# Performance work log

Measured on AMD Instinct MI355X. Metric: run time of the kernel, lower is better.

## Reference

```python
import jax, jax.numpy as jnp
import numpy as np

B, T, H, V = 32, 256, 1024, 256


def setup_inputs() -> dict:
    key = jax.random.key(0)
    ks = jax.random.split(key, 12)
    xavier = float(np.sqrt(6.0 / (H + V)))
    inp = {
        "x": jax.random.randint(ks[0], (B, T), 0, V, dtype=jnp.int64),
        "targets": jax.random.randint(ks[1], (B, T), 0, V, dtype=jnp.int64),
        "h0": jnp.zeros((B, H), jnp.float32),
        "c0": jnp.zeros((B, H), jnp.float32),
        "h1": jnp.zeros((B, H), jnp.float32),
        "c1": jnp.zeros((B, H), jnp.float32),
        # learned params
        "emb": jax.random.normal(ks[2], (V, H), jnp.float32) * 0.05,
        "W_ih0": jax.random.normal(ks[3], (H, 4 * H), jnp.float32) / np.sqrt(H),
        "W_hh0": jax.random.normal(ks[4], (H, 4 * H), jnp.float32) / np.sqrt(H),
        "b0": jnp.zeros((4 * H,), jnp.float32),
        "W_ih1": jax.random.normal(ks[5], (H, 4 * H), jnp.float32) / np.sqrt(H),
        "W_hh1": jax.random.normal(ks[6], (H, 4 * H), jnp.float32) / np.sqrt(H),
        "b1": jnp.zeros((4 * H,), jnp.float32),
        "W_out": jax.random.uniform(ks[7], (H, V), jnp.float32, -xavier, xavier),
        "b_out": jnp.zeros((V,), jnp.float32),
    }
    return inp


def _lstm_cell(h, c, inp, W_ih, W_hh, b):
    # gates: [B, 4H] -> i, f, g, o
    z = inp @ W_ih + h @ W_hh + b
    i, f, g, o = jnp.split(z, 4, axis=-1)
    c_new = jax.nn.sigmoid(f) * c + jax.nn.sigmoid(i) * jnp.tanh(g)
    h_new = jax.nn.sigmoid(o) * jnp.tanh(c_new)
    return h_new, c_new


def reference(x, targets, h0, c0, h1, c1, emb, W_ih0, W_hh0, b0,
              W_ih1, W_hh1, b1, W_out, b_out):
    # Teacher-forcing branch: embed targets, feed embedding at every step.
    embeddings = emb[targets]            # [B, T, H]
    e_seq = jnp.swapaxes(embeddings, 0, 1)  # [T, B, H] for scan over time

    def step(carry, e_t):
        (h0, c0), (h1, c1) = carry
        h0, c0 = _lstm_cell(h0, c0, e_t, W_ih0, W_hh0, b0)
        h1, c1 = _lstm_cell(h1, c1, h0, W_ih1, W_hh1, b1)
        logit = h1 @ W_out + b_out       # [B, V]
        return ((h0, c0), (h1, c1)), logit

    carry0 = ((h0, c0), (h1, c1))
    carry_f, logits_tbv = jax.lax.scan(step, carry0, e_seq)
    logits = jnp.swapaxes(logits_tbv, 0, 1)  # [B, T, V]
    (h0f, c0f), (h1f, c1f) = carry_f
    return logits, h0f, c0f, h1f, c1f
```

## Files before the change

### kernel.cpp

```cpp
#include <hip/hip_runtime.h>
#include <cstdint>


typedef float  f32x4 __attribute__((ext_vector_type(4)));
typedef short  s16x8 __attribute__((ext_vector_type(8)));

#define DEV __device__ __forceinline__

DEV unsigned short f2bf(float x){
  unsigned u = __builtin_bit_cast(unsigned, x);
  unsigned r = (u + 0x7fffu + ((u >> 16) & 1u)) >> 16;
  return (unsigned short)r;
}
DEV float bf2f(unsigned short b){ return __builtin_bit_cast(float, ((unsigned)b) << 16); }

DEV s16x8 ld16(const void* p){ return *(const s16x8*)p; }

DEV f32x4 MF(s16x8 a, s16x8 b, f32x4 c){
  return __builtin_amdgcn_mfma_f32_16x16x32_bf16(a, b, c, 0, 0, 0);
}

#define LDC(dst, ptr)  asm volatile("global_load_dwordx4 %0, %1, off sc0 sc1" : "=v"(dst) : "v"(ptr))
#define LDC4(dst, ptr) asm volatile("global_load_dwordx4 %0, %1, off sc0 sc1" : "=v"(dst) : "v"(ptr))
#define LDP(dst, ptr)  asm volatile("global_load_dwordx4 %0, %1, off"         : "=v"(dst) : "v"(ptr))
#define WAITVM(n) do { asm volatile("s_waitcnt vmcnt(" #n ")" ::: "memory"); \
                       __builtin_amdgcn_sched_barrier(0); } while (0)
#define TRIPLE(Cmn, Ahm, Alm, Bhn, Bln) do { \
    Cmn = MF(Ahm, Bhn, Cmn); Cmn = MF(Ahm, Bln, Cmn); Cmn = MF(Alm, Bhn, Cmn); } while (0)

DEV void st2c(void* p, unsigned short v){
  asm volatile("global_store_short %0, %1, off sc0 sc1" :: "v"(p), "v"((unsigned)v) : "memory");
}
DEV void set_flag(int* p, int v){
  __hip_atomic_store(p, v, __ATOMIC_RELAXED, __HIP_MEMORY_SCOPE_AGENT);
}
DEV void poll2(const int* f, int lane, int target){
  const int* p0 = f + lane * 8;
  const int* p1 = f + (64 + lane) * 8;
  for (;;) {
    int a = __hip_atomic_load(p0, __ATOMIC_RELAXED, __HIP_MEMORY_SCOPE_AGENT);
    int b = __hip_atomic_load(p1, __ATOMIC_RELAXED, __HIP_MEMORY_SCOPE_AGENT);
    if (__all((a >= target) && (b >= target))) break;
    __builtin_amdgcn_s_sleep(1);
  }
}
DEV char* h0slot(char* wa0, char* s0, char* hi, int s){
  return (s == 0) ? s0 : ((s <= 128) ? wa0 + ((size_t)(s - 1) << 17)
                                     : hi  + ((size_t)(s - 129) << 17));
}

__global__ void prep_wfrag(const float* __restrict__ W0, const float* __restrict__ W1,
                           const float* __restrict__ W2, const float* __restrict__ W3,
                           char* D0, char* D1, char* D2, char* D3) {
  int gid = blockIdx.x * 256 + threadIdx.x;
  int lane = gid & 63, ks = (gid >> 6) & 31, jb = (gid >> 11) & 255, mat = gid >> 19;
  const float* S = (mat == 0) ? W0 : (mat == 1) ? W1 : (mat == 2) ? W2 : W3;
  char* D = (mat == 0) ? D0 : (mat == 1) ? D1 : (mat == 2) ? D2 : D3;
  int jp = jb * 16 + (lane & 15), u = jp >> 2, g = jp & 3;
  int kb = ks * 32 + (lane >> 4) * 8;
  s16x8 vh, vl;
  #pragma unroll
  for (int i = 0; i < 8; ++i) {
    float x = S[(kb + i) * 4096 + g * 1024 + u];
    unsigned short h = f2bf(x);
    vh[i] = (short)h;
    vl[i] = (short)f2bf(x - bf2f(h));
  }
  *(s16x8*)(D + (((jb * 2 + 0) * 32 + ks) << 10) + lane * 16) = vh;
  *(s16x8*)(D + (((jb * 2 + 1) * 32 + ks) << 10) + lane * 16) = vl;
}

__global__ void prep_bfrag(const float* __restrict__ emb, const float* __restrict__ Wout,
                           char* Demb, char* Dwout) {
  int gid = blockIdx.x * 256 + threadIdx.x;
  int lane = gid & 63, ks = (gid >> 6) & 31, vb = (gid >> 11) & 15, which = gid >> 15;
  int v = vb * 16 + (lane & 15), kb = ks * 32 + (lane >> 4) * 8;
  s16x8 vh, vl;
  #pragma unroll
  for (int i = 0; i < 8; ++i) {
    float x = which ? Wout[(kb + i) * 256 + v] : emb[v * 1024 + kb + i];
    unsigned short h = f2bf(x);
    vh[i] = (short)h;
    vl[i] = (short)f2bf(x - bf2f(h));
  }
  char* D = which ? Dwout : Demb;
  *(s16x8*)(D + (((vb * 2 + 0) * 32 + ks) << 10) + lane * 16) = vh;
  *(s16x8*)(D + (((vb * 2 + 1) * 32 + ks) << 10) + lane * 16) = vl;
}

__global__ void prep_hinit(const float* __restrict__ h0, const float* __restrict__ h1,
                           char* h0s0, char* h1f) {
  int gid = blockIdx.x * 256 + threadIdx.x;
  int lane = gid & 63, ks = (gid >> 6) & 31, nt = (gid >> 11) & 1, which = gid >> 12;
  const float* S = which ? h1 : h0;
  char* D = which ? h1f : h0s0;
  int b = nt * 16 + (lane & 15), kb = ks * 32 + (lane >> 4) * 8;
  s16x8 vh, vl;
  #pragma unroll
  for (int i = 0; i < 8; ++i) {
    float x = S[b * 1024 + kb + i];
    unsigned short h = f2bf(x);
    vh[i] = (short)h;
    vl[i] = (short)f2bf(x - bf2f(h));
  }
  *(s16x8*)(D + (((0 * 2 + nt) * 32 + ks) << 10) + lane * 16) = vh;
  *(s16x8*)(D + (((1 * 2 + nt) * 32 + ks) << 10) + lane * 16) = vl;
}

__global__ void prep_misc(const float* __restrict__ b1, float* b1i, int* f0a, int* f1a) {
  int i = blockIdx.x * 256 + threadIdx.x;
  if (i < 4096) b1i[i] = b1[(i & 3) * 1024 + (i >> 2)];
  if (i < 1024) { f0a[i] = -1; f1a[i] = -1; }
}

__global__ __launch_bounds__(256, 1) void lstm_persist(
    const int* __restrict__ tgt,
    const float* __restrict__ c0_in, const float* __restrict__ c1_in,
    const float* __restrict__ b0, const float* __restrict__ b_out,
    char* __restrict__ WA0, const char* __restrict__ WA1, const char* __restrict__ WA2,
    const char* __restrict__ WAi0, const char* __restrict__ WoutB, const char* __restrict__ embB,
    float* __restrict__ E0, const float* __restrict__ b1i,
    char* __restrict__ h0s0, char* __restrict__ h0hi, char* __restrict__ h1frag,
    int* __restrict__ f0, int* __restrict__ f1,
    float* __restrict__ out)
{
  extern __shared__ char smem[];
  const int tid = threadIdx.x, lane = tid & 63, wv = tid >> 6;
  const int wg = blockIdx.x;
  const bool isL0 = (wg < 128);
  const int wgl = isL0 ? wg : (wg - 128);
  const int l15 = lane & 15, l4 = lane >> 4;

  __builtin_amdgcn_fence(__ATOMIC_ACQUIRE, "agent");

  if (isL0) {
    uint4 tmp[8];
    for (int blk = 0; blk < 4; ++blk) {
      #pragma unroll
      for (int q = 0; q < 8; ++q) {
        int idx = tid + (blk * 8 + q) * 256;
        int l16 = idx & 63, ks = (idx >> 6) & 31, mi = (idx >> 11) & 1, part = idx >> 12;
        LDC4(tmp[q], WA0 + ((((wgl * 2 + mi) * 2 + part) * 32 + ks) << 10) + l16 * 16);
      }
      WAITVM(0);
      #pragma unroll
      for (int q = 0; q < 8; ++q) {
        int idx = tid + (blk * 8 + q) * 256;
        int l16 = idx & 63, ks = (idx >> 6) & 31, mi = (idx >> 11) & 1, part = idx >> 12;
        *(uint4*)(smem + (((part * 2 + mi) * 32 + ks) << 10) + l16 * 16) = tmp[q];
      }
    }
  } else {
    for (int idx = tid; idx < 8192; idx += 256) {
      int l16 = idx & 63, ks = (idx >> 6) & 31, mi = (idx >> 11) & 1, mat = idx >> 12;
      const char* W = mat ? WA2 : WA1;
      uint4 v = *(const uint4*)(W + ((((wgl * 2 + mi) * 2 + 0) * 32 + ks) << 10) + l16 * 16);
      *(uint4*)(smem + (((mat * 2 + mi) * 32 + ks) << 10) + l16 * 16) = v;
    }
  }

  if (isL0) {
    f32x4 C[2][4];
    #pragma unroll
    for (int a = 0; a < 2; ++a)
      #pragma unroll
      for (int b = 0; b < 4; ++b) C[a][b] = 0.0f;
    for (int ks = 0; ks < 32; ++ks) {
      s16x8 Ah0, Ah1, Al0, Al1;
      LDC(Ah0, WAi0 + ((((wgl * 2 + 0) * 2 + 0) * 32 + ks) << 10) + lane * 16);
      LDC(Ah1, WAi0 + ((((wgl * 2 + 1) * 2 + 0) * 32 + ks) << 10) + lane * 16);
      LDC(Al0, WAi0 + ((((wgl * 2 + 0) * 2 + 1) * 32 + ks) << 10) + lane * 16);
      LDC(Al1, WAi0 + ((((wgl * 2 + 1) * 2 + 1) * 32 + ks) << 10) + lane * 16);
      WAITVM(0);
      #pragma unroll
      for (int v4 = 0; v4 < 4; ++v4) {
        int vb = wv * 4 + v4;
        s16x8 Bh = ld16(embB + (((vb * 2 + 0) * 32 + ks) << 10) + lane * 16);
        s16x8 Bl = ld16(embB + (((vb * 2 + 1) * 32 + ks) << 10) + lane * 16);
        TRIPLE(C[0][v4], Ah0, Al0, Bh, Bl);
        TRIPLE(C[1][v4], Ah1, Al1, Bh, Bl);
      }
    }
    #pragma unroll
    for (int mi = 0; mi < 2; ++mi) {
      int jb4 = wgl * 32 + mi * 16 + l4 * 4;
      int u = jb4 >> 2;
      f32x4 bb;
      #pragma unroll
      for (int r = 0; r < 4; ++r) bb[r] = b0[r * 1024 + u];
      #pragma unroll
      for (int v4 = 0; v4 < 4; ++v4) {
        int v = (wv * 4 + v4) * 16 + l15;
        *(f32x4*)(E0 + v * 4096 + jb4) = C[mi][v4] + bb;
      }
    }
  }

  float cst[2];
  if (wv < 2) {
    const float* cs = isL0 ? c0_in : c1_in;
    #pragma unroll
    for (int nt = 0; nt < 2; ++nt)
      cst[nt] = cs[(nt * 16 + l15) * 1024 + wgl * 8 + wv * 4 + l4];
  }
  __syncthreads();
  if (tid == 0) set_flag((isL0 ? f0 : f1) + wgl * 8, 0);

  for (int t = 0; t < 256; ++t) {
    const int s = t + 1;
    f32x4 C[2][2];
    #pragma unroll
    for (int a = 0; a < 2; ++a)
      #pragma unroll
      for (int b = 0; b < 2; ++b) C[a][b] = 0.0f;

    if (isL0) {
      if (wv == 0) poll2(f0, lane, t);
      __syncthreads();
      const char* Bb = h0slot(WA0, h0s0, h0hi, t);
      const int ksb = wv * 8;
      s16x8 P[3][4];
      #pragma unroll
      for (int q = 0; q < 4; ++q) LDP(P[0][q], Bb + ((q * 32 + ksb) << 10) + lane * 16);
      #pragma unroll
      for (int q = 0; q < 4; ++q) LDP(P[1][q], Bb + ((q * 32 + ksb + 1) << 10) + lane * 16);
      #pragma unroll
      for (int i = 0; i < 8; ++i) {
        const int ks = ksb + i;
        if (i < 6) {
          #pragma unroll
          for (int q = 0; q < 4; ++q) LDP(P[(i + 2) % 3][q], Bb + ((q * 32 + ks + 2) << 10) + lane * 16);
        }
        s16x8 Ah0 = ld16(smem + ((0 * 32 + ks) << 10) + lane * 16);
        s16x8 Ah1 = ld16(smem + ((1 * 32 + ks) << 10) + lane * 16);
        s16x8 Al0 = ld16(smem + ((2 * 32 + ks) << 10) + lane * 16);
        s16x8 Al1 = ld16(smem + ((3 * 32 + ks) << 10) + lane * 16);
        if (i < 6) { WAITVM(8); } else if (i == 6) { WAITVM(4); } else { WAITVM(0); }
        TRIPLE(C[0][0], Ah0, Al0, P[i % 3][0], P[i % 3][2]);
        TRIPLE(C[0][1], Ah0, Al0, P[i % 3][1], P[i % 3][3]);
        TRIPLE(C[1][0], Ah1, Al1, P[i % 3][0], P[i % 3][2]);
        TRIPLE(C[1][1], Ah1, Al1, P[i % 3][1], P[i % 3][3]);
      }
    } else {
      if (wv == 0) poll2(f1, lane, t);
      __syncthreads();
      {
        const char* Bb = h1frag + (size_t)t * 131072;
        const int ksb = wv * 8;
        s16x8 P[3][4], AL[3][2];
        #pragma unroll
        for (int d = 0; d < 2; ++d) {
          #pragma unroll
          for (int q = 0; q < 4; ++q) LDP(P[d][q], Bb + ((q * 32 + ksb + d) << 10) + lane * 16);
          LDP(AL[d][0], WA2 + ((((wgl * 2 + 0) * 2 + 1) * 32 + ksb + d) << 10) + lane * 16);
          LDP(AL[d][1], WA2 + ((((wgl * 2 + 1) * 2 + 1) * 32 + ksb + d) << 10) + lane * 16);
        }
        #pragma unroll
        for (int i = 0; i < 8; ++i) {
          const int ks = ksb + i;
          if (i < 6) {
            #pragma unroll
            for (int q = 0; q < 4; ++q) LDP(P[(i + 2) % 3][q], Bb + ((q * 32 + ks + 2) << 10) + lane * 16);
            LDP(AL[(i + 2) % 3][0], WA2 + ((((wgl * 2 + 0) * 2 + 1) * 32 + ks + 2) << 10) + lane * 16);
            LDP(AL[(i + 2) % 3][1], WA2 + ((((wgl * 2 + 1) * 2 + 1) * 32 + ks + 2) << 10) + lane * 16);
          }
          s16x8 Ah0 = ld16(smem + (((2 + 0) * 32 + ks) << 10) + lane * 16);
          s16x8 Ah1 = ld16(smem + (((2 + 1) * 32 + ks) << 10) + lane * 16);
          if (i < 6) { WAITVM(12); } else if (i == 6) { WAITVM(6); } else { WAITVM(0); }
          TRIPLE(C[0][0], Ah0, AL[i % 3][0], P[i % 3][0], P[i % 3][2]);
          TRIPLE(C[0][1], Ah0, AL[i % 3][0], P[i % 3][1], P[i % 3][3]);
          TRIPLE(C[1][0], Ah1, AL[i % 3][1], P[i % 3][0], P[i % 3][2]);
          TRIPLE(C[1][1], Ah1, AL[i % 3][1], P[i % 3][1], P[i % 3][3]);
        }
      }
      if (wv == 0) poll2(f0, lane, s);
      __syncthreads();
      {
        const char* Bb = h0slot(WA0, h0s0, h0hi, s);
        const int ksb = wv * 8;
        s16x8 P[3][4], AL[3][2];
        #pragma unroll
        for (int d = 0; d < 2; ++d) {
          #pragma unroll
          for (int q = 0; q < 4; ++q) LDP(P[d][q], Bb + ((q * 32 + ksb + d) << 10) + lane * 16);
          LDP(AL[d][0], WA1 + ((((wgl * 2 + 0) * 2 + 1) * 32 + ksb + d) << 10) + lane * 16);
          LDP(AL[d][1], WA1 + ((((wgl * 2 + 1) * 2 + 1) * 32 + ksb + d) << 10) + lane * 16);
        }
        #pragma unroll
        for (int i = 0; i < 8; ++i) {
          const int ks = ksb + i;
          if (i < 6) {
            #pragma unroll
            for (int q = 0; q < 4; ++q) LDP(P[(i + 2) % 3][q], Bb + ((q * 32 + ks + 2) << 10) + lane * 16);
            LDP(AL[(i + 2) % 3][0], WA1 + ((((wgl * 2 + 0) * 2 + 1) * 32 + ks + 2) << 10) + lane * 16);
            LDP(AL[(i + 2) % 3][1], WA1 + ((((wgl * 2 + 1) * 2 + 1) * 32 + ks + 2) << 10) + lane * 16);
          }
          s16x8 Ah0 = ld16(smem + (((0 + 0) * 32 + ks) << 10) + lane * 16);
          s16x8 Ah1 = ld16(smem + (((0 + 1) * 32 + ks) << 10) + lane * 16);
          if (i < 6) { WAITVM(12); } else if (i == 6) { WAITVM(6); } else { WAITVM(0); }
          TRIPLE(C[0][0], Ah0, AL[i % 3][0], P[i % 3][0], P[i % 3][2]);
          TRIPLE(C[0][1], Ah0, AL[i % 3][0], P[i % 3][1], P[i % 3][3]);
          TRIPLE(C[1][0], Ah1, AL[i % 3][1], P[i % 3][0], P[i % 3][2]);
          TRIPLE(C[1][1], Ah1, AL[i % 3][1], P[i % 3][1], P[i % 3][3]);
        }
      }
    }

    #pragma unroll
    for (int mi = 0; mi < 2; ++mi)
      #pragma unroll
      for (int nt = 0; nt < 2; ++nt)
        *(f32x4*)(smem + 131072 + ((wv * 4 + mi * 2 + nt) << 10) + lane * 16) = C[mi][nt];
    __syncthreads();

    if (wv < 2) {
      const int mi = wv;
      char* hd = isL0 ? h0slot(WA0, h0s0, h0hi, s)
                      : (h1frag + (size_t)s * 131072);
      #pragma unroll
      for (int nt = 0; nt < 2; ++nt) {
        f32x4 z = {0.f, 0.f, 0.f, 0.f};
        #pragma unroll
        for (int p = 0; p < 4; ++p)
          z += *(const f32x4*)(smem + 131072 + ((p * 4 + mi * 2 + nt) << 10) + lane * 16);
        if (isL0) {
          int tv = tgt[(nt * 16 + l15) * 256 + t];
          z += *(const f32x4*)(E0 + tv * 4096 + wgl * 32 + mi * 16 + l4 * 4);
        } else {
          z += *(const f32x4*)(b1i + wgl * 32 + mi * 16 + l4 * 4);
        }
        float ig = 1.f / (1.f + __expf(-z[0]));
        float fg = 1.f / (1.f + __expf(-z[1]));
        float og = 1.f / (1.f + __expf(-z[3]));
        float cn = fg * cst[nt] + ig * tanhf(z[2]);
        float hn = og * tanhf(cn);
        cst[nt] = cn;
        unsigned short hb = f2bf(hn);
        unsigned short lb = f2bf(hn - bf2f(hb));
        int base = ((0 * 2 + nt) * 32 + (wgl >> 2)) * 1024 + ((wgl & 3) * 16 + l15) * 16 + (mi * 4 + l4) * 2;
        st2c(hd + base, hb);
        st2c(hd + base + 65536, lb);
        if (t == 255) {
          int u = wgl * 8 + mi * 4 + l4, b = nt * 16 + l15;
          int off = isL0 ? 0 : 65536;
          out[2097152 + off + b * 1024 + u] = hn;
          out[2097152 + off + 32768 + b * 1024 + u] = cn;
        }
      }
      asm volatile("s_waitcnt vmcnt(0)" ::: "memory");
    }
    __syncthreads();
    if (tid == 0) set_flag((isL0 ? f0 : f1) + wgl * 8, s);
  }

  {
    const int tp = isL0 ? (128 + wgl) : wgl;
    if (wv == 0) poll2(f1, lane, tp + 1);
    __syncthreads();
    const char* A = h1frag + (size_t)(tp + 1) * 131072;
    f32x4 C[2][4];
    #pragma unroll
    for (int a = 0; a < 2; ++a)
      #pragma unroll
      for (int b = 0; b < 4; ++b) C[a][b] = 0.0f;
    s16x8 QA[4], QB[4];
    #pragma unroll
    for (int q = 0; q < 4; ++q) LDP(QA[q], A + ((q * 32 + 0) << 10) + lane * 16);
    for (int kk = 0; kk < 16; ++kk) {
      const int ks = kk * 2;
      #pragma unroll
      for (int q = 0; q < 4; ++q) LDP(QB[q], A + ((q * 32 + ks + 1) << 10) + lane * 16);
      asm volatile("s_waitcnt vmcnt(4)" ::: "memory");
      __builtin_amdgcn_sched_barrier(0);
      #pragma unroll
      for (int v4 = 0; v4 < 4; ++v4) {
        int vb = wv * 4 + v4;
        s16x8 Bh = ld16(WoutB + (((vb * 2 + 0) * 32 + ks) << 10) + lane * 16);
        s16x8 Bl = ld16(WoutB + (((vb * 2 + 1) * 32 + ks) << 10) + lane * 16);
        C[0][v4] = MF(QA[0], Bh, C[0][v4]); C[0][v4] = MF(QA[0], Bl, C[0][v4]); C[0][v4] = MF(QA[2], Bh, C[0][v4]);
        C[1][v4] = MF(QA[1], Bh, C[1][v4]); C[1][v4] = MF(QA[1], Bl, C[1][v4]); C[1][v4] = MF(QA[3], Bh, C[1][v4]);
      }
      if (kk < 15) {
        #pragma unroll
        for (int q = 0; q < 4; ++q) LDP(QA[q], A + ((q * 32 + ks + 2) << 10) + lane * 16);
        asm volatile("s_waitcnt vmcnt(4)" ::: "memory");
      } else {
        asm volatile("s_waitcnt vmcnt(0)" ::: "memory");
      }
      __builtin_amdgcn_sched_barrier(0);
      #pragma unroll
      for (int v4 = 0; v4 < 4; ++v4) {
        int vb = wv * 4 + v4;
        s16x8 Bh = ld16(WoutB + (((vb * 2 + 0) * 32 + ks + 1) << 10) + lane * 16);
        s16x8 Bl = ld16(WoutB + (((vb * 2 + 1) * 32 + ks + 1) << 10) + lane * 16);
        C[0][v4] = MF(QB[0], Bh, C[0][v4]); C[0][v4] = MF(QB[0], Bl, C[0][v4]); C[0][v4] = MF(QB[2], Bh, C[0][v4]);
        C[1][v4] = MF(QB[1], Bh, C[1][v4]); C[1][v4] = MF(QB[1], Bl, C[1][v4]); C[1][v4] = MF(QB[3], Bh, C[1][v4]);
      }
    }
    #pragma unroll
    for (int nt = 0; nt < 2; ++nt)
      #pragma unroll
      for (int v4 = 0; v4 < 4; ++v4) {
        int v = (wv * 4 + v4) * 16 + l15;
        float bo = b_out[v];
        #pragma unroll
        for (int r = 0; r < 4; ++r) {
          int b = nt * 16 + l4 * 4 + r;
          out[((size_t)b * 256 + tp) * 256 + v] = C[nt][v4][r] + bo;
        }
      }
  }
}

extern "C" void kernel_launch(void* const* d_in, const int* in_sizes, int n_in,
                              void* d_out, int out_size, void* d_ws, size_t ws_size,
                              hipStream_t stream) {
  const int*   targets = (const int*)d_in[1];
  const float* h0_in   = (const float*)d_in[2];
  const float* c0_in   = (const float*)d_in[3];
  const float* h1_in   = (const float*)d_in[4];
  const float* c1_in   = (const float*)d_in[5];
  const float* emb     = (const float*)d_in[6];
  const float* W_ih0   = (const float*)d_in[7];
  const float* W_hh0   = (const float*)d_in[8];
  const float* b0      = (const float*)d_in[9];
  const float* W_ih1   = (const float*)d_in[10];
  const float* W_hh1   = (const float*)d_in[11];
  const float* b1      = (const float*)d_in[12];
  const float* W_out   = (const float*)d_in[13];
  const float* b_out   = (const float*)d_in[14];
  float* out = (float*)d_out;

  char* ws = (char*)d_ws;
  char*  WA0    = ws;
  char*  WA1    = ws + 16777216;
  char*  WA2    = ws + 33554432;
  char*  WoutB  = ws + 50331648;
  char*  embB   = ws + 51380224;
  float* E0     = (float*)(ws + 52428800);
  float* b1i    = (float*)(ws + 56623104);
  int*   f0     = (int*)(ws + 56639488);
  int*   f1     = (int*)(ws + 56643584);
  char*  h0s0   = ws + 56647680;
  char*  h0hi   = ws + 56778752;
  char*  h1frag = ws + 73555968;
  char*  WAi0   = h1frag + 16777216;

  prep_misc <<<18,   256, 0, stream>>>(b1, b1i, f0, f1);
  prep_wfrag<<<8192, 256, 0, stream>>>(W_hh0, W_ih1, W_hh1, W_ih0, WA0, WA1, WA2, WAi0);
  prep_bfrag<<<256,  256, 0, stream>>>(emb, W_out, embB, WoutB);
  prep_hinit<<<32,   256, 0, stream>>>(h0_in, h1_in, h0s0, h1frag);

  hipFuncSetAttribute(reinterpret_cast<const void*>(lstm_persist),
                      hipFuncAttributeMaxDynamicSharedMemorySize, 147456);
  lstm_persist<<<256, 256, 147456, stream>>>(
      targets, c0_in, c1_in, b0, b_out,
      WA0, WA1, WA2, WAi0, WoutB, embB,
      E0, b1i, h0s0, h0hi, h1frag, f0, f1, out);
}
```

Before: 2.126 ms.

## Split layer-1 waves across recurrent/input GEMMs and coalesce h stores via LDS

Layer-1 workgroups now split the work by wave: two waves compute the W_hh1·h1 product and two compute the W_ih1·h0 product concurrently, each over 16 k-steps, in place of running the two phases back to back. Every wave polls the flags itself, which drops a block barrier before each phase. The gate nonlinearity is spread over all four waves. The resulting bf16 hi/lo h values are staged in LDS and written with one 16-byte coherent store per lane in place of many 2-byte stores. The embedding-gate row is prefetched before polling. Risks are extra flag-polling traffic from all waves and a little more shared memory.

```diff
diff --git a/kernel.cpp b/kernel.cpp
--- a/kernel.cpp
+++ b/kernel.cpp
@@ -2,8 +2,9 @@
 #include <cstdint>
 
 
-typedef float  f32x4 __attribute__((ext_vector_type(4)));
-typedef short  s16x8 __attribute__((ext_vector_type(8)));
+typedef float    f32x4 __attribute__((ext_vector_type(4)));
+typedef short    s16x8 __attribute__((ext_vector_type(8)));
+typedef unsigned u32x4 __attribute__((ext_vector_type(4)));
 
 #define DEV __device__ __forceinline__
 
@@ -21,15 +22,15 @@
 }
 
 #define LDC(dst, ptr)  asm volatile("global_load_dwordx4 %0, %1, off sc0 sc1" : "=v"(dst) : "v"(ptr))
-#define LDC4(dst, ptr) asm volatile("global_load_dwordx4 %0, %1, off sc0 sc1" : "=v"(dst) : "v"(ptr))
 #define LDP(dst, ptr)  asm volatile("global_load_dwordx4 %0, %1, off"         : "=v"(dst) : "v"(ptr))
 #define WAITVM(n) do { asm volatile("s_waitcnt vmcnt(" #n ")" ::: "memory"); \
                        __builtin_amdgcn_sched_barrier(0); } while (0)
+#define CFENCE()  asm volatile("" ::: "memory")
 #define TRIPLE(Cmn, Ahm, Alm, Bhn, Bln) do { \
     Cmn = MF(Ahm, Bhn, Cmn); Cmn = MF(Ahm, Bln, Cmn); Cmn = MF(Alm, Bhn, Cmn); } while (0)
 
-DEV void st2c(void* p, unsigned short v){
-  asm volatile("global_store_short %0, %1, off sc0 sc1" :: "v"(p), "v"((unsigned)v) : "memory");
+DEV void st16c(void* p, u32x4 v){
+  asm volatile("global_store_dwordx4 %0, %1, off sc0 sc1" :: "v"(p), "v"(v) : "memory");
 }
 DEV void set_flag(int* p, int v){
   __hip_atomic_store(p, v, __ATOMIC_RELAXED, __HIP_MEMORY_SCOPE_AGENT);
@@ -43,6 +44,7 @@
     if (__all((a >= target) && (b >= target))) break;
     __builtin_amdgcn_s_sleep(1);
   }
+  CFENCE();
 }
 DEV char* h0slot(char* wa0, char* s0, char* hi, int s){
   return (s == 0) ? s0 : ((s <= 128) ? wa0 + ((size_t)(s - 1) << 17)
@@ -125,37 +127,40 @@
     float* __restrict__ out)
 {
   extern __shared__ char smem[];
+  constexpr int PART = 131072;
+  constexpr int RP   = 131072 + 16384;
   const int tid = threadIdx.x, lane = tid & 63, wv = tid >> 6;
   const int wg = blockIdx.x;
   const bool isL0 = (wg < 128);
   const int wgl = isL0 ? wg : (wg - 128);
   const int l15 = lane & 15, l4 = lane >> 4;
+  const int mi_e = wv >> 1, nt_e = wv & 1;
 
   __builtin_amdgcn_fence(__ATOMIC_ACQUIRE, "agent");
 
   if (isL0) {
-    uint4 tmp[8];
+    u32x4 tmp[8];
     for (int blk = 0; blk < 4; ++blk) {
       #pragma unroll
       for (int q = 0; q < 8; ++q) {
         int idx = tid + (blk * 8 + q) * 256;
         int l16 = idx & 63, ks = (idx >> 6) & 31, mi = (idx >> 11) & 1, part = idx >> 12;
-        LDC4(tmp[q], WA0 + ((((wgl * 2 + mi) * 2 + part) * 32 + ks) << 10) + l16 * 16);
+        LDC(tmp[q], WA0 + ((((wgl * 2 + mi) * 2 + part) * 32 + ks) << 10) + l16 * 16);
       }
       WAITVM(0);
       #pragma unroll
       for (int q = 0; q < 8; ++q) {
         int idx = tid + (blk * 8 + q) * 256;
         int l16 = idx & 63, ks = (idx >> 6) & 31, mi = (idx >> 11) & 1, part = idx >> 12;
-        *(uint4*)(smem + (((part * 2 + mi) * 32 + ks) << 10) + l16 * 16) = tmp[q];
+        *(u32x4*)(smem + (((part * 2 + mi) * 32 + ks) << 10) + l16 * 16) = tmp[q];
       }
     }
   } else {
     for (int idx = tid; idx < 8192; idx += 256) {
       int l16 = idx & 63, ks = (idx >> 6) & 31, mi = (idx >> 11) & 1, mat = idx >> 12;
       const char* W = mat ? WA2 : WA1;
-      uint4 v = *(const uint4*)(W + ((((wgl * 2 + mi) * 2 + 0) * 32 + ks) << 10) + l16 * 16);
-      *(uint4*)(smem + (((mat * 2 + mi) * 32 + ks) << 10) + l16 * 16) = v;
+      u32x4 v = *(const u32x4*)(W + ((((wgl * 2 + mi) * 2 + 0) * 32 + ks) << 10) + l16 * 16);
+      *(u32x4*)(smem + (((mat * 2 + mi) * 32 + ks) << 10) + l16 * 16) = v;
     }
   }
 
@@ -196,13 +201,14 @@
     }
   }
 
-  float cst[2];
-  if (wv < 2) {
+  float cst;
+  {
     const float* cs = isL0 ? c0_in : c1_in;
-    #pragma unroll
-    for (int nt = 0; nt < 2; ++nt)
-      cst[nt] = cs[(nt * 16 + l15) * 1024 + wgl * 8 + wv * 4 + l4];
-  }
+    cst = cs[(nt_e * 16 + l15) * 1024 + wgl * 8 + mi_e * 4 + l4];
+  }
+  f32x4 b1z = {0.f, 0.f, 0.f, 0.f};
+  if (!isL0) b1z = *(const f32x4*)(b1i + wgl * 32 + mi_e * 16 + (l4 << 2));
+
   __syncthreads();
   if (tid == 0) set_flag((isL0 ? f0 : f1) + wgl * 8, 0);
 
@@ -214,16 +220,19 @@
       #pragma unroll
       for (int b = 0; b < 2; ++b) C[a][b] = 0.0f;
 
+    f32x4 e0v = {0.f, 0.f, 0.f, 0.f};
+
     if (isL0) {
-      if (wv == 0) poll2(f0, lane, t);
-      __syncthreads();
+      int tv = tgt[(nt_e * 16 + l15) * 256 + t];
+      e0v = *(const f32x4*)(E0 + (size_t)tv * 4096 + wgl * 32 + mi_e * 16 + (l4 << 2));
+      poll2(f0, lane, t);
       const char* Bb = h0slot(WA0, h0s0, h0hi, t);
       const int ksb = wv * 8;
       s16x8 P[3][4];
       #pragma unroll
-      for (int q = 0; q < 4; ++q) LDP(P[0][q], Bb + ((q * 32 + ksb) << 10) + lane * 16);
-      #pragma unroll
-      for (int q = 0; q < 4; ++q) LDP(P[1][q], Bb + ((q * 32 + ksb + 1) << 10) + lane * 16);
+      for (int d = 0; d < 2; ++d)
+        #pragma unroll
+        for (int q = 0; q < 4; ++q) LDP(P[d][q], Bb + ((q * 32 + ksb + d) << 10) + lane * 16);
       #pragma unroll
       for (int i = 0; i < 8; ++i) {
         const int ks = ksb + i;
@@ -242,67 +251,36 @@
         TRIPLE(C[1][1], Ah1, Al1, P[i % 3][1], P[i % 3][3]);
       }
     } else {
-      if (wv == 0) poll2(f1, lane, t);
-      __syncthreads();
-      {
-        const char* Bb = h1frag + (size_t)t * 131072;
-        const int ksb = wv * 8;
-        s16x8 P[3][4], AL[3][2];
+      const int mat = (wv < 2) ? 1 : 0;
+      if (wv < 2) poll2(f1, lane, t); else poll2(f0, lane, s);
+      const char* Bb  = (wv < 2) ? (h1frag + (size_t)t * 131072)
+                                 : h0slot(WA0, h0s0, h0hi, s);
+      const char* ALb = (wv < 2) ? WA2 : WA1;
+      const int ksb = (wv & 1) * 16;
+      s16x8 P[3][4], AL[3][2];
+      #pragma unroll
+      for (int d = 0; d < 2; ++d) {
         #pragma unroll
-        for (int d = 0; d < 2; ++d) {
+        for (int q = 0; q < 4; ++q) LDP(P[d][q], Bb + ((q * 32 + ksb + d) << 10) + lane * 16);
+        LDP(AL[d][0], ALb + ((((wgl * 2 + 0) * 2 + 1) * 32 + ksb + d) << 10) + lane * 16);
+        LDP(AL[d][1], ALb + ((((wgl * 2 + 1) * 2 + 1) * 32 + ksb + d) << 10) + lane * 16);
+      }
+      #pragma unroll
+      for (int i = 0; i < 16; ++i) {
+        const int ks = ksb + i;
+        if (i < 14) {
           #pragma unroll
-          for (int q = 0; q < 4; ++q) LDP(P[d][q], Bb + ((q * 32 + ksb + d) << 10) + lane * 16);
-          LDP(AL[d][0], WA2 + ((((wgl * 2 + 0) * 2 + 1) * 32 + ksb + d) << 10) + lane * 16);
-          LDP(AL[d][1], WA2 + ((((wgl * 2 + 1) * 2 + 1) * 32 + ksb + d) << 10) + lane * 16);
+          for (int q = 0; q < 4; ++q) LDP(P[(i + 2) % 3][q], Bb + ((q * 32 + ks + 2) << 10) + lane * 16);
+          LDP(AL[(i + 2) % 3][0], ALb + ((((wgl * 2 + 0) * 2 + 1) * 32 + ks + 2) << 10) + lane * 16);
+          LDP(AL[(i + 2) % 3][1], ALb + ((((wgl * 2 + 1) * 2 + 1) * 32 + ks + 2) << 10) + lane * 16);
         }
-        #pragma unroll
-        for (int i = 0; i < 8; ++i) {
-          const int ks = ksb + i;
-          if (i < 6) {
-            #pragma unroll
-            for (int q = 0; q < 4; ++q) LDP(P[(i + 2) % 3][q], Bb + ((q * 32 + ks + 2) << 10) + lane * 16);
-            LDP(AL[(i + 2) % 3][0], WA2 + ((((wgl * 2 + 0) * 2 + 1) * 32 + ks + 2) << 10) + lane * 16);
-            LDP(AL[(i + 2) % 3][1], WA2 + ((((wgl * 2 + 1) * 2 + 1) * 32 + ks + 2) << 10) + lane * 16);
-          }
-          s16x8 Ah0 = ld16(smem + (((2 + 0) * 32 + ks) << 10) + lane * 16);
-          s16x8 Ah1 = ld16(smem + (((2 + 1) * 32 + ks) << 10) + lane * 16);
-          if (i < 6) { WAITVM(12); } else if (i == 6) { WAITVM(6); } else { WAITVM(0); }
-          TRIPLE(C[0][0], Ah0, AL[i % 3][0], P[i % 3][0], P[i % 3][2]);
-          TRIPLE(C[0][1], Ah0, AL[i % 3][0], P[i % 3][1], P[i % 3][3]);
-          TRIPLE(C[1][0], Ah1, AL[i % 3][1], P[i % 3][0], P[i % 3][2]);
-          TRIPLE(C[1][1], Ah1, AL[i % 3][1], P[i % 3][1], P[i % 3][3]);
-        }
-      }
-      if (wv == 0) poll2(f0, lane, s);
-      __syncthreads();
-      {
-        const char* Bb = h0slot(WA0, h0s0, h0hi, s);
-        const int ksb = wv * 8;
-        s16x8 P[3][4], AL[3][2];
-        #pragma unroll
-        for (int d = 0; d < 2; ++d) {
-          #pragma unroll
-          for (int q = 0; q < 4; ++q) LDP(P[d][q], Bb + ((q * 32 + ksb + d) << 10) + lane * 16);
-          LDP(AL[d][0], WA1 + ((((wgl * 2 + 0) * 2 + 1) * 32 + ksb + d) << 10) + lane * 16);
-          LDP(AL[d][1], WA1 + ((((wgl * 2 + 1) * 2 + 1) * 32 + ksb + d) << 10) + lane * 16);
-        }
-        #pragma unroll
-        for (int i = 0; i < 8; ++i) {
-          const int ks = ksb + i;
-          if (i < 6) {
-            #pragma unroll
-            for (int q = 0; q < 4; ++q) LDP(P[(i + 2) % 3][q], Bb + ((q * 32 + ks + 2) << 10) + lane * 16);
-            LDP(AL[(i + 2) % 3][0], WA1 + ((((wgl * 2 + 0) * 2 + 1) * 32 + ks + 2) << 10) + lane * 16);
-            LDP(AL[(i + 2) % 3][1], WA1 + ((((wgl * 2 + 1) * 2 + 1) * 32 + ks + 2) << 10) + lane * 16);
-          }
-          s16x8 Ah0 = ld16(smem + (((0 + 0) * 32 + ks) << 10) + lane * 16);
-          s16x8 Ah1 = ld16(smem + (((0 + 1) * 32 + ks) << 10) + lane * 16);
-          if (i < 6) { WAITVM(12); } else if (i == 6) { WAITVM(6); } else { WAITVM(0); }
-          TRIPLE(C[0][0], Ah0, AL[i % 3][0], P[i % 3][0], P[i % 3][2]);
-          TRIPLE(C[0][1], Ah0, AL[i % 3][0], P[i % 3][1], P[i % 3][3]);
-          TRIPLE(C[1][0], Ah1, AL[i % 3][1], P[i % 3][0], P[i % 3][2]);
-          TRIPLE(C[1][1], Ah1, AL[i % 3][1], P[i % 3][1], P[i % 3][3]);
-        }
+        s16x8 Ah0 = ld16(smem + (((mat * 2 + 0) * 32 + ks) << 10) + lane * 16);
+        s16x8 Ah1 = ld16(smem + (((mat * 2 + 1) * 32 + ks) << 10) + lane * 16);
+        if (i < 14) { WAITVM(12); } else if (i == 14) { WAITVM(6); } else { WAITVM(0); }
+        TRIPLE(C[0][0], Ah0, AL[i % 3][0], P[i % 3][0], P[i % 3][2]);
+        TRIPLE(C[0][1], Ah0, AL[i % 3][0], P[i % 3][1], P[i % 3][3]);
+        TRIPLE(C[1][0], Ah1, AL[i % 3][1], P[i % 3][0], P[i % 3][2]);
+        TRIPLE(C[1][1], Ah1, AL[i % 3][1], P[i % 3][1], P[i % 3][3]);
       }
     }
 
@@ -310,53 +288,48 @@
     for (int mi = 0; mi < 2; ++mi)
       #pragma unroll
       for (int nt = 0; nt < 2; ++nt)
-        *(f32x4*)(smem + 131072 + ((wv * 4 + mi * 2 + nt) << 10) + lane * 16) = C[mi][nt];
+        *(f32x4*)(smem + PART + ((wv * 4 + mi * 2 + nt) << 10) + lane * 16) = C[mi][nt];
     __syncthreads();
 
-    if (wv < 2) {
-      const int mi = wv;
+    {
+      f32x4 z = *(const f32x4*)(smem + PART + ((0 * 4 + wv) << 10) + lane * 16);
+      #pragma unroll
+      for (int w = 1; w < 4; ++w)
+        z += *(const f32x4*)(smem + PART + ((w * 4 + wv) << 10) + lane * 16);
+      z += isL0 ? e0v : b1z;
+      float ig = 1.f / (1.f + __expf(-z[0]));
+      float fg = 1.f / (1.f + __expf(-z[1]));
+      float og = 1.f / (1.f + __expf(-z[3]));
+      float cn = fg * cst + ig * tanhf(z[2]);
+      float hn = og * tanhf(cn);
+      cst = cn;
+      unsigned short hb = f2bf(hn);
+      unsigned short lb = f2bf(hn - bf2f(hb));
+      *(short*)(smem + RP + ((0 + nt_e) * 16 + l15) * 16 + (mi_e * 4 + l4) * 2) = (short)hb;
+      *(short*)(smem + RP + ((2 + nt_e) * 16 + l15) * 16 + (mi_e * 4 + l4) * 2) = (short)lb;
+      if (t == 255) {
+        int u = wgl * 8 + mi_e * 4 + l4, b = nt_e * 16 + l15;
+        int off = isL0 ? 0 : 65536;
+        out[2097152 + off + b * 1024 + u] = hn;
+        out[2097152 + off + 32768 + b * 1024 + u] = cn;
+      }
+    }
+    __syncthreads();
+
+    if (wv == 0) {
       char* hd = isL0 ? h0slot(WA0, h0s0, h0hi, s)
                       : (h1frag + (size_t)s * 131072);
-      #pragma unroll
-      for (int nt = 0; nt < 2; ++nt) {
-        f32x4 z = {0.f, 0.f, 0.f, 0.f};
-        #pragma unroll
-        for (int p = 0; p < 4; ++p)
-          z += *(const f32x4*)(smem + 131072 + ((p * 4 + mi * 2 + nt) << 10) + lane * 16);
-        if (isL0) {
-          int tv = tgt[(nt * 16 + l15) * 256 + t];
-          z += *(const f32x4*)(E0 + tv * 4096 + wgl * 32 + mi * 16 + l4 * 4);
-        } else {
-          z += *(const f32x4*)(b1i + wgl * 32 + mi * 16 + l4 * 4);
-        }
-        float ig = 1.f / (1.f + __expf(-z[0]));
-        float fg = 1.f / (1.f + __expf(-z[1]));
-        float og = 1.f / (1.f + __expf(-z[3]));
-        float cn = fg * cst[nt] + ig * tanhf(z[2]);
-        float hn = og * tanhf(cn);
-        cst[nt] = cn;
-        unsigned short hb = f2bf(hn);
-        unsigned short lb = f2bf(hn - bf2f(hb));
-        int base = ((0 * 2 + nt) * 32 + (wgl >> 2)) * 1024 + ((wgl & 3) * 16 + l15) * 16 + (mi * 4 + l4) * 2;
-        st2c(hd + base, hb);
-        st2c(hd + base + 65536, lb);
-        if (t == 255) {
-          int u = wgl * 8 + mi * 4 + l4, b = nt * 16 + l15;
-          int off = isL0 ? 0 : 65536;
-          out[2097152 + off + b * 1024 + u] = hn;
-          out[2097152 + off + 32768 + b * 1024 + u] = cn;
-        }
-      }
+      u32x4 v = *(const u32x4*)(smem + RP + lane * 16);
+      char* dst = hd + (((lane >> 4) * 32 + (wgl >> 2)) << 10) + ((wgl & 3) * 16 + l15) * 16;
+      st16c(dst, v);
       asm volatile("s_waitcnt vmcnt(0)" ::: "memory");
-    }
-    __syncthreads();
-    if (tid == 0) set_flag((isL0 ? f0 : f1) + wgl * 8, s);
+      if (lane == 0) set_flag((isL0 ? f0 : f1) + wgl * 8, s);
+    }
   }
 
   {
     const int tp = isL0 ? (128 + wgl) : wgl;
-    if (wv == 0) poll2(f1, lane, tp + 1);
-    __syncthreads();
+    poll2(f1, lane, tp + 1);
     const char* A = h1frag + (size_t)(tp + 1) * 131072;
     f32x4 C[2][4];
     #pragma unroll
@@ -452,8 +425,8 @@
   prep_hinit<<<32,   256, 0, stream>>>(h0_in, h1_in, h0s0, h1frag);
 
   hipFuncSetAttribute(reinterpret_cast<const void*>(lstm_persist),
-                      hipFuncAttributeMaxDynamicSharedMemorySize, 147456);
-  lstm_persist<<<256, 256, 147456, stream>>>(
+                      hipFuncAttributeMaxDynamicSharedMemorySize, 148480);
+  lstm_persist<<<256, 256, 148480, stream>>>(
       targets, c0_in, c1_in, b0, b_out,
       WA0, WA1, WA2, WAi0, WoutB, embB,
       E0, b1i, h0s0, h0hi, h1frag, f0, f1, out);
```

Result: faster. 1.873 ms (-11.9%).
